# Performance work log

Hardware: AMD Instinct MI355X
Metric: run time of the kernel (lower is better)

## Reference

```python
import jax, jax.numpy as jnp
import numpy as np

NUM_HEADS = 16
BN_EPS = 1e-3  # tf.layers.BatchNormalization default epsilon


def _z_norm(a, axis, scale):
    mu = jnp.mean(a, axis=axis, keepdims=True)
    sd = jnp.std(a, axis=axis, keepdims=True)
    return (a - mu) / (sd * scale + 1e-10)


def setup_inputs() -> dict:
    key = jax.random.key(0)
    ks = jax.random.split(key, 12)
    B, S, D = 4, 1024, 1024
    w = lambda k: jax.random.normal(k, (D, D), dtype=jnp.float32) * 0.02
    return {
        'q': jax.random.normal(ks[0], (B, S, D), dtype=jnp.float32),
        'k': jax.random.normal(ks[1], (B, S, D), dtype=jnp.float32),
        'v': jax.random.normal(ks[2], (B, S, D), dtype=jnp.float32),
        'mask': jax.random.randint(ks[3], (B, 1, S, S), 0, 2, dtype=jnp.int32),
        'is_training': 0,
        'q_gamma': jnp.ones((D,), jnp.float32),
        'q_beta': jnp.zeros((D,), jnp.float32),
        'q_mean': jax.random.normal(ks[4], (D,), dtype=jnp.float32) * 0.1,
        'q_var': jnp.ones((D,), jnp.float32),
        'Wq': w(ks[5]), 'bq': jnp.zeros((D,), jnp.float32),
        'Wqq': w(ks[6]), 'bqq': jnp.zeros((D,), jnp.float32),
        'Wo': w(ks[7]), 'bo': jnp.zeros((D,), jnp.float32),
    }


def reference(q, k, v, mask, is_training, q_gamma, q_beta, q_mean, q_var,
              Wq, bq, Wqq, bqq, Wo, bo):
    B, S, D = q.shape
    H = NUM_HEADS
    dh = D // H
    # BatchNorm (inference mode: call() passes no training flag -> moving stats)
    x = (q - q_mean) * jax.lax.rsqrt(q_var + BN_EPS) * q_gamma + q_beta
    # q = wqq(relu(wq(.)))  (k/v projections are dead: call() sets k = v = q)
    x = jax.nn.relu(x @ Wq + bq)
    x = x @ Wqq + bqq
    qh = x.reshape(B, S, H, dh).transpose(0, 2, 1, 3)  # [B,H,S,dh]
    logits = jnp.einsum('bhqd,bhkd->bhqk', qh, qh) / jnp.sqrt(jnp.float32(dh))
    logits = logits + mask.astype(logits.dtype) * -1e9
    attn = jax.nn.softmax(logits, axis=3)  # [B,H,S,S]
    last = jnp.mean(logits, axis=-1, keepdims=True)        # [B,H,S,1]
    last2 = jnp.mean(logits, axis=(2, 3), keepdims=True)   # [B,H,1,1]
    w_within = jax.nn.softmax(_z_norm(last, 2, 2), axis=2)   # softmax over queries
    w_betw = jax.nn.softmax(_z_norm(last2, 1, 2), axis=1)    # softmax over heads
    attn = attn * w_within * w_betw
    out = jnp.einsum('bhqk,bhkd->bhqd', attn, qh)           # v == qh
    out = out.transpose(0, 2, 1, 3).reshape(B, S, D)
    out = out @ Wo + bo
    return out, attn
```

## Files before the change

kernel.cpp:

```cpp
#include <hip/hip_runtime.h>
#include <math.h>


constexpr int Bz = 4, S = 1024, D = 1024, H = 16, DH = 64;
constexpr int N_ROWS = Bz * S;
#define BN_EPS 1e-3f
#define NEG_BIG -1e9f

typedef __attribute__((ext_vector_type(8))) short bf16x8;
typedef __attribute__((ext_vector_type(8))) unsigned short u16x8;
typedef __attribute__((ext_vector_type(4))) float f32x4;

__device__ inline unsigned short f2bf(float f) {
  union { float f; unsigned int u; } v; v.f = f;
  unsigned int u = v.u;
  return (unsigned short)((u + 0x7FFFu + ((u >> 16) & 1u)) >> 16);
}
__device__ inline float bf2f(unsigned short h) {
  union { unsigned int u; float f; } v; v.u = ((unsigned int)h) << 16;
  return v.f;
}
__device__ inline bf16x8 pack8(float4 a, float4 b) {
  bf16x8 v;
  v[0] = (short)f2bf(a.x); v[1] = (short)f2bf(a.y);
  v[2] = (short)f2bf(a.z); v[3] = (short)f2bf(a.w);
  v[4] = (short)f2bf(b.x); v[5] = (short)f2bf(b.y);
  v[6] = (short)f2bf(b.z); v[7] = (short)f2bf(b.w);
  return v;
}
__device__ inline float4 bnf(float4 f, float4 s, float4 sh) {
  return make_float4(fmaf(f.x, s.x, sh.x), fmaf(f.y, s.y, sh.y),
                     fmaf(f.z, s.z, sh.z), fmaf(f.w, s.w, sh.w));
}

__device__ __forceinline__ void gl16(const void* g, void* l) {
  __builtin_amdgcn_global_load_lds(
      (const __attribute__((address_space(1))) unsigned int*)(unsigned long long)g,
      (__attribute__((address_space(3))) unsigned int*)(unsigned int)(unsigned long long)l,
      16, 0, 0);
}

__global__ __launch_bounds__(256)
void k_prep_all(const float* __restrict__ W0, const float* __restrict__ W1,
                const float* __restrict__ W2, unsigned short* __restrict__ T0,
                unsigned short* __restrict__ T1, unsigned short* __restrict__ T2,
                const float* __restrict__ gamma, const float* __restrict__ beta,
                const float* __restrict__ mean, const float* __restrict__ var,
                float* __restrict__ bnsc, float* __restrict__ bnsh,
                const int* __restrict__ mask, float* __restrict__ n_cnt2,
                float* __restrict__ cs) {
  __shared__ float Ls[64][65];
  const int bid = blockIdx.x, t = threadIdx.x;
  if (bid < 768) {
    const int z = bid >> 8, rem = bid & 255;
    const float* W = z == 0 ? W0 : (z == 1 ? W1 : W2);
    unsigned short* T = z == 0 ? T0 : (z == 1 ? T1 : T2);
    const int k0 = (rem & 15) * 64, n0 = (rem >> 4) * 64;
    {
      const int r = t >> 2, c0 = (t & 3) * 16;
#pragma unroll
      for (int i = 0; i < 4; ++i) {
        float4 f = *(const float4*)&W[(size_t)(k0 + r) * 1024 + n0 + c0 + 4 * i];
        Ls[r][c0 + 4 * i] = f.x; Ls[r][c0 + 4 * i + 1] = f.y;
        Ls[r][c0 + 4 * i + 2] = f.z; Ls[r][c0 + 4 * i + 3] = f.w;
      }
    }
    __syncthreads();
    {
      const int d = t >> 2, c = t & 3;
      u16x8 o0, o1;
#pragma unroll
      for (int i = 0; i < 8; ++i) {
        o0[i] = f2bf(Ls[c * 16 + i][d]);
        o1[i] = f2bf(Ls[c * 16 + 8 + i][d]);
      }
      unsigned short* dst = &T[(size_t)(n0 + d) * 1024 + k0 + c * 16];
      *(u16x8*)dst = o0;
      *(u16x8*)(dst + 8) = o1;
    }
  } else if (bid < 832) {
    const int id = bid - 768;
    const int row = id * 64 + (t >> 2);
    const int4* mp = (const int4*)&mask[(size_t)row * 1024 + (t & 3) * 256];
    int s = 0;
#pragma unroll 8
    for (int i = 0; i < 64; ++i) { int4 m = mp[i]; s += (m.x + m.y) + (m.z + m.w); }
    s += __shfl_xor(s, 1, 64);
    s += __shfl_xor(s, 2, 64);
    if ((t & 3) == 0) n_cnt2[row] = (float)s;
  } else if (bid < 836) {
    const int id = bid - 832;
    *(float4*)&cs[id * 1024 + t * 4] = make_float4(0.f, 0.f, 0.f, 0.f);
  } else {
    const int i = (bid - 836) * 256 + t;
    float sc = gamma[i] * rsqrtf(var[i] + BN_EPS);
    bnsc[i] = sc;
    bnsh[i] = beta[i] - mean[i] * sc;
  }
}

template<int AMODE, bool RELU, bool OUTBF, bool CSUM>
__global__ __launch_bounds__(256)
void k_gemm2n(const void* __restrict__ Asrc, const unsigned short* __restrict__ BT,
              const float* __restrict__ bias, void* __restrict__ C,
              const float* __restrict__ bnsc, const float* __restrict__ bnsh,
              float* __restrict__ cs) {
  __shared__ unsigned short As[128 * 64];
  __shared__ unsigned short Bs[64 * 64];
  const int t = threadIdx.x;
  const int w = t >> 6, l = t & 63, l15 = l & 15, l4 = l >> 4;
  const int m0 = blockIdx.x * 128, n0 = blockIdx.y * 64;
  const int wm = (w >> 1) * 64, wn = (w & 1) * 32;

  f32x4 acc[4][2];
#pragma unroll
  for (int i = 0; i < 4; ++i)
#pragma unroll
    for (int j = 0; j < 2; ++j) acc[i][j] = (f32x4){0.f, 0.f, 0.f, 0.f};

  for (int k0 = 0; k0 < 1024; k0 += 64) {
    __syncthreads();
#pragma unroll
    for (int i = 0; i < 4; ++i) {
      const int c = i * 256 + t, row = c >> 3, slot = c & 7;
      if (AMODE == 0) {
        const char* gs = (const char*)&((const unsigned short*)Asrc)[(size_t)(m0 + row) * 1024 + k0] +
                         ((slot * 16) ^ ((row & 7) << 4));
        gl16(gs, (char*)As + (i * 256 + w * 64) * 16);
      } else {
        const float* ap = &((const float*)Asrc)[(size_t)(m0 + row) * 1024 + k0 + slot * 8];
        float4 f0 = *(const float4*)ap, f1 = *(const float4*)(ap + 4);
        float4 s0 = *(const float4*)&bnsc[k0 + slot * 8];
        float4 s1 = *(const float4*)&bnsc[k0 + slot * 8 + 4];
        float4 h0 = *(const float4*)&bnsh[k0 + slot * 8];
        float4 h1 = *(const float4*)&bnsh[k0 + slot * 8 + 4];
        bf16x8 v = pack8(bnf(f0, s0, h0), bnf(f1, s1, h1));
        *(bf16x8*)((char*)As + row * 128 + ((slot * 16) ^ ((row & 7) << 4))) = v;
      }
    }
#pragma unroll
    for (int i = 0; i < 2; ++i) {
      const int c = i * 256 + t, row = c >> 3, slot = c & 7;
      const char* gs = (const char*)&BT[(size_t)(n0 + row) * 1024 + k0] +
                       ((slot * 16) ^ ((row & 7) << 4));
      gl16(gs, (char*)Bs + (i * 256 + w * 64) * 16);
    }
    __syncthreads();
    bf16x8 af[4][2], bfr[2][2];
#pragma unroll
    for (int bm = 0; bm < 4; ++bm) {
      const int r = wm + bm * 16 + l15;
#pragma unroll
      for (int kk = 0; kk < 2; ++kk)
        af[bm][kk] = *(const bf16x8*)((const char*)As + r * 128 +
                                      ((kk * 64 + l4 * 16) ^ ((r & 7) << 4)));
    }
#pragma unroll
    for (int bn = 0; bn < 2; ++bn) {
      const int r = wn + bn * 16 + l15;
#pragma unroll
      for (int kk = 0; kk < 2; ++kk)
        bfr[bn][kk] = *(const bf16x8*)((const char*)Bs + r * 128 +
                                       ((kk * 64 + l4 * 16) ^ ((r & 7) << 4)));
    }
#pragma unroll
    for (int bm = 0; bm < 4; ++bm)
#pragma unroll
      for (int bn = 0; bn < 2; ++bn) {
        acc[bm][bn] = __builtin_amdgcn_mfma_f32_16x16x32_bf16(af[bm][0], bfr[bn][0], acc[bm][bn], 0, 0, 0);
        acc[bm][bn] = __builtin_amdgcn_mfma_f32_16x16x32_bf16(af[bm][1], bfr[bn][1], acc[bm][bn], 0, 0, 0);
      }
  }
  float bv[2];
#pragma unroll
  for (int bn = 0; bn < 2; ++bn) bv[bn] = bias[n0 + wn + bn * 16 + l15];
  float csum[2] = {0.f, 0.f};
#pragma unroll
  for (int bm = 0; bm < 4; ++bm)
#pragma unroll
    for (int bn = 0; bn < 2; ++bn)
#pragma unroll
      for (int r = 0; r < 4; ++r) {
        float v = acc[bm][bn][r] + bv[bn];
        if (RELU) v = fmaxf(v, 0.f);
        if (CSUM) csum[bn] += v;
        const size_t idx = (size_t)(m0 + wm + bm * 16 + l4 * 4 + r) * 1024 +
                           n0 + wn + bn * 16 + l15;
        if (OUTBF) ((unsigned short*)C)[idx] = f2bf(v);
        else ((float*)C)[idx] = v;
      }
  if (CSUM) {
#pragma unroll
    for (int bn = 0; bn < 2; ++bn) {
      float s = csum[bn];
      s += __shfl_xor(s, 16, 64);
      s += __shfl_xor(s, 32, 64);
      if (l4 == 0)
        atomicAdd(&cs[(m0 >> 10) * 1024 + n0 + wn + bn * 16 + l15], s);
    }
  }
}

__global__ __launch_bounds__(256)
void k_cvt(const unsigned short* __restrict__ xqb, unsigned short* __restrict__ qhT) {
  __shared__ unsigned short Ls[64][72];
  const int t = threadIdx.x;
  const int b = blockIdx.x >> 4;
  const int sb = (blockIdx.x & 15) * 64;
  const int h = blockIdx.y;
  {
    const int r = t >> 2, c0 = (t & 3) * 16;
    const unsigned short* src = &xqb[(size_t)(b * 1024 + sb + r) * 1024 + h * 64 + c0];
    u16x8 a = *(const u16x8*)src;
    u16x8 b8 = *(const u16x8*)(src + 8);
    *(u16x8*)&Ls[r][c0] = a;
    *(u16x8*)&Ls[r][c0 + 8] = b8;
  }
  __syncthreads();
  {
    const int d = t >> 2, c = t & 3;
    u16x8 o0, o1;
#pragma unroll
    for (int i = 0; i < 8; ++i) {
      o0[i] = Ls[c * 16 + i][d];
      o1[i] = Ls[c * 16 + 8 + i][d];
    }
    unsigned short* dst = &qhT[(size_t)((b * 16 + h) * 64 + d) * 1024 + sb + c * 16];
    *(u16x8*)dst = o0;
    *(u16x8*)(dst + 8) = o1;
  }
}

template<int PASS>
__global__ __launch_bounds__(256)
void k_attn6(const unsigned short* __restrict__ xqb, const int* __restrict__ mask,
             const unsigned short* __restrict__ qhT, const float* __restrict__ w_row,
             float* __restrict__ attn, unsigned short* __restrict__ pvb,
             float* __restrict__ denom) {
  __shared__ unsigned short Ks[2][128 * 64];
  __shared__ unsigned short Pst[PASS ? 4 * 16 * 64 : 8];

  const int t = threadIdx.x;
  const int w = t >> 6, l = t & 63;
  const int l15 = l & 15, l4 = l >> 4;
  const int q0 = blockIdx.x * 64;
  const int h = blockIdx.y, b = blockIdx.z;
  const int bh = b * 16 + h;

  bf16x8 qa0, qa1;
  {
    const unsigned short* qp =
        &xqb[(size_t)(b * 1024 + q0 + w * 16 + l15) * 1024 + h * 64 + l4 * 8];
    qa0 = *(const bf16x8*)qp;
    qa1 = *(const bf16x8*)(qp + 32);
  }

  float wsc[4];
  if (PASS == 1) {
#pragma unroll
    for (int r = 0; r < 4; ++r)
      wsc[r] = w_row[(size_t)bh * 1024 + q0 + w * 16 + l4 * 4 + r];
  }

  float dsum[4] = {0.f, 0.f, 0.f, 0.f};
  f32x4 vacc[4];
#pragma unroll
  for (int c = 0; c < 4; ++c) vacc[c] = (f32x4){0.f, 0.f, 0.f, 0.f};

#pragma unroll
  for (int i = 0; i < 4; ++i) {
    const int c = i * 256 + t, row = c >> 3, slot = c & 7;
    const char* gs = (const char*)&xqb[(size_t)(b * 1024 + row) * 1024 + h * 64] +
                     ((slot * 16) ^ ((row & 7) << 4));
    gl16(gs, (char*)Ks[0] + (i * 256 + w * 64) * 16);
  }

  for (int ti = 0; ti < 8; ++ti) {
    __syncthreads();
    const int cur = ti & 1;
    if (ti < 7) {
#pragma unroll
      for (int i = 0; i < 4; ++i) {
        const int c = i * 256 + t, row = c >> 3, slot = c & 7;
        const char* gs = (const char*)&xqb[(size_t)(b * 1024 + (ti + 1) * 128 + row) * 1024 + h * 64] +
                         ((slot * 16) ^ ((row & 7) << 4));
        gl16(gs, (char*)Ks[cur ^ 1] + (i * 256 + w * 64) * 16);
      }
    }
    const int k0 = ti * 128;

#pragma unroll
    for (int half = 0; half < 2; ++half) {
      const int koff = k0 + half * 64;
      f32x4 lacc[4];
#pragma unroll
      for (int c = 0; c < 4; ++c) {
        const int r = half * 64 + c * 16 + l15;
        const char* kb = (const char*)Ks[cur] + r * 128;
        const int rsw = (r & 7) << 4;
        bf16x8 kb0 = *(const bf16x8*)(kb + ((l4 * 16) ^ rsw));
        bf16x8 kb1 = *(const bf16x8*)(kb + ((64 + l4 * 16) ^ rsw));
        f32x4 z = (f32x4){0.f, 0.f, 0.f, 0.f};
        z = __builtin_amdgcn_mfma_f32_16x16x32_bf16(qa0, kb0, z, 0, 0, 0);
        z = __builtin_amdgcn_mfma_f32_16x16x32_bf16(qa1, kb1, z, 0, 0, 0);
        lacc[c] = z;
      }

      int mrr[4][4];
#pragma unroll
      for (int c = 0; c < 4; ++c)
#pragma unroll
        for (int r = 0; r < 4; ++r)
          mrr[c][r] = mask[(size_t)(b * 1024 + q0 + w * 16 + l4 * 4 + r) * 1024 +
                           koff + c * 16 + l15];

#pragma unroll
      for (int c = 0; c < 4; ++c) {
#pragma unroll
        for (int r = 0; r < 4; ++r) {
          float p = __expf(fmaf((float)mrr[c][r], NEG_BIG, lacc[c][r] * 0.125f));
          if (PASS == 0) {
            dsum[r] += p;
          } else {
            attn[(size_t)(bh * 1024 + q0 + w * 16 + l4 * 4 + r) * 1024 +
                 koff + c * 16 + l15] = p * wsc[r];
            const int qq = l4 * 4 + r;
            *(unsigned short*)((char*)&Pst[w * 1024] + qq * 128 +
                               (((c * 16 + l15) * 2) ^ ((qq & 7) << 4))) = f2bf(p);
          }
        }
      }

      if (PASS == 1) {
#pragma unroll
        for (int kk = 0; kk < 2; ++kk) {
          const char* pb = (const char*)&Pst[w * 1024] + l15 * 128;
          bf16x8 pa = *(const bf16x8*)(pb + ((kk * 64 + l4 * 16) ^ ((l15 & 7) << 4)));
#pragma unroll
          for (int c = 0; c < 4; ++c) {
            bf16x8 vb = *(const bf16x8*)&qhT[(size_t)(bh * 64 + c * 16 + l15) * 1024 +
                                             koff + kk * 32 + l4 * 8];
            vacc[c] = __builtin_amdgcn_mfma_f32_16x16x32_bf16(pa, vb, vacc[c], 0, 0, 0);
          }
        }
      }
    }
  }

  if (PASS == 0) {
#pragma unroll
    for (int r = 0; r < 4; ++r) {
      float d2 = dsum[r];
#pragma unroll
      for (int m = 1; m < 16; m <<= 1) d2 += __shfl_xor(d2, m, 64);
      if (l15 == 0)
        denom[(size_t)bh * 1024 + q0 + w * 16 + l4 * 4 + r] = d2;
    }
  } else {
#pragma unroll
    for (int c = 0; c < 4; ++c)
#pragma unroll
      for (int r = 0; r < 4; ++r)
        pvb[(size_t)(b * 1024 + q0 + w * 16 + l4 * 4 + r) * 1024 +
            h * 64 + c * 16 + l15] = f2bf(vacc[c][r] * wsc[r]);
  }
}

__global__ __launch_bounds__(256)
void k_wwithin(const unsigned short* __restrict__ xqb, const float* __restrict__ cs,
               const float* __restrict__ n_cnt2, const float* __restrict__ denom,
               float* __restrict__ w_row) {
  __shared__ double buf[1024];
  __shared__ double red[256];
  __shared__ float csl[64];
  __shared__ double sh_mu, sh_sd, sh_zm, sh_es;
  const int bh = blockIdx.x, t = threadIdx.x;
  const int base = bh << 10;
  const int b = bh >> 4, h = bh & 15;
  const int nbase = b << 10;
  if (t < 64) csl[t] = cs[b * 1024 + h * 64 + t];
  __syncthreads();
  double part = 0;
  for (int j = 0; j < 4; ++j) {
    const int q2 = t + j * 256;
    const unsigned short* xr = &xqb[(size_t)(b * 1024 + q2) * 1024 + h * 64];
    float s = 0.f;
#pragma unroll
    for (int dd = 0; dd < 64; dd += 8) {
      u16x8 xv = *(const u16x8*)&xr[dd];
      s += bf2f(xv[0]) * csl[dd]     + bf2f(xv[1]) * csl[dd + 1] +
           bf2f(xv[2]) * csl[dd + 2] + bf2f(xv[3]) * csl[dd + 3] +
           bf2f(xv[4]) * csl[dd + 4] + bf2f(xv[5]) * csl[dd + 5] +
           bf2f(xv[6]) * csl[dd + 6] + bf2f(xv[7]) * csl[dd + 7];
    }
    double last = ((double)(s * 0.125f) - 1e9 * (double)n_cnt2[nbase + q2]) * (1.0 / 1024.0);
    buf[q2] = last; part += last;
  }
  red[t] = part; __syncthreads();
  for (int s2 = 128; s2 > 0; s2 >>= 1) { if (t < s2) red[t] += red[t + s2]; __syncthreads(); }
  if (t == 0) sh_mu = red[0] * (1.0 / 1024.0);
  __syncthreads();
  const double mu = sh_mu;
  part = 0;
  for (int q2 = t; q2 < 1024; q2 += 256) { double d = buf[q2] - mu; part += d * d; }
  red[t] = part; __syncthreads();
  for (int s2 = 128; s2 > 0; s2 >>= 1) { if (t < s2) red[t] += red[t + s2]; __syncthreads(); }
  if (t == 0) sh_sd = sqrt(red[0] * (1.0 / 1024.0));
  __syncthreads();
  const double dn = sh_sd * 2.0 + 1e-10;
  part = -1e300;
  for (int q2 = t; q2 < 1024; q2 += 256) {
    double z = (buf[q2] - mu) / dn;
    buf[q2] = z;
    part = fmax(part, z);
  }
  red[t] = part; __syncthreads();
  for (int s2 = 128; s2 > 0; s2 >>= 1) { if (t < s2) red[t] = fmax(red[t], red[t + s2]); __syncthreads(); }
  if (t == 0) sh_zm = red[0];
  __syncthreads();
  const double zm = sh_zm;
  part = 0;
  for (int q2 = t; q2 < 1024; q2 += 256) {
    double e = exp(buf[q2] - zm);
    buf[q2] = e; part += e;
  }
  red[t] = part; __syncthreads();
  for (int s2 = 128; s2 > 0; s2 >>= 1) { if (t < s2) red[t] += red[t + s2]; __syncthreads(); }
  if (t == 0) sh_es = red[0];
  __syncthreads();
  const double tot = sh_es;
  for (int q2 = t; q2 < 1024; q2 += 256) {
    w_row[base + q2] = (float)(buf[q2] / tot * 0.0625 / (double)denom[base + q2]);
  }
}

extern "C" void kernel_launch(void* const* d_in, const int* in_sizes, int n_in,
                              void* d_out, int out_size, void* d_ws, size_t ws_size,
                              hipStream_t stream) {
  const float* q      = (const float*)d_in[0];
  const int*   mask   = (const int*)d_in[3];
  const float* q_gamma = (const float*)d_in[5];
  const float* q_beta  = (const float*)d_in[6];
  const float* q_mean  = (const float*)d_in[7];
  const float* q_var   = (const float*)d_in[8];
  const float* Wq  = (const float*)d_in[9];
  const float* bq  = (const float*)d_in[10];
  const float* Wqq = (const float*)d_in[11];
  const float* bqq = (const float*)d_in[12];
  const float* Wo  = (const float*)d_in[13];
  const float* bo  = (const float*)d_in[14];

  float* out  = (float*)d_out;
  float* attn = (float*)d_out + (size_t)N_ROWS * D;
  unsigned short* xqb = (unsigned short*)d_out;

  char* ws = (char*)d_ws;
  unsigned short* x1b = (unsigned short*)(ws);
  unsigned short* qhT = (unsigned short*)(ws + (8u << 20));
  unsigned short* pvb = (unsigned short*)(ws + (16u << 20));
  unsigned short* WqT  = (unsigned short*)(ws + (32u << 20));
  unsigned short* WqqT = (unsigned short*)(ws + (34u << 20));
  unsigned short* WoT  = (unsigned short*)(ws + (36u << 20));
  float* cs     = (float*)(ws + (38u << 20));
  float* denom  = cs + 4096;
  float* w_row  = denom + 65536;
  float* n_cnt2 = w_row + 65536;
  float* bnsc   = n_cnt2 + 4096;
  float* bnsh   = bnsc + 1024;

  k_prep_all<<<840, 256, 0, stream>>>(Wq, Wqq, Wo, WqT, WqqT, WoT,
                                      q_gamma, q_beta, q_mean, q_var, bnsc, bnsh,
                                      mask, n_cnt2, cs);

  dim3 gg(32, 16);
  k_gemm2n<1, true, true, false><<<gg, 256, 0, stream>>>(q, WqT, bq, x1b, bnsc, bnsh, nullptr);
  k_gemm2n<0, false, true, true><<<gg, 256, 0, stream>>>(x1b, WqqT, bqq, xqb, nullptr, nullptr, cs);

  k_cvt<<<dim3(64, 16), 256, 0, stream>>>(xqb, qhT);

  dim3 ga(16, 16, 4);
  k_attn6<0><<<ga, 256, 0, stream>>>(xqb, mask, nullptr, nullptr, nullptr, nullptr, denom);
  k_wwithin<<<Bz * H, 256, 0, stream>>>(xqb, cs, n_cnt2, denom, w_row);
  k_attn6<1><<<ga, 256, 0, stream>>>(xqb, mask, qhT, w_row, attn, pvb, nullptr);

  k_gemm2n<0, false, false, false><<<gg, 256, 0, stream>>>(pvb, WoT, bo, out, nullptr, nullptr, nullptr);
}
```

Baseline: 246.4 us.

## Materialize bf16 softmax numerators in pass one and reuse them for the attn write and PV

```diff
diff --git a/kernel.cpp b/kernel.cpp
--- a/kernel.cpp
+++ b/kernel.cpp
@@ -231,14 +231,11 @@
   }
 }
 
-template<int PASS>
 __global__ __launch_bounds__(256)
-void k_attn6(const unsigned short* __restrict__ xqb, const int* __restrict__ mask,
-             const unsigned short* __restrict__ qhT, const float* __restrict__ w_row,
-             float* __restrict__ attn, unsigned short* __restrict__ pvb,
-             float* __restrict__ denom) {
+void k_attn7(const unsigned short* __restrict__ xqb, const int* __restrict__ mask,
+             unsigned short* __restrict__ pbuf, float* __restrict__ denom) {
   __shared__ unsigned short Ks[2][128 * 64];
-  __shared__ unsigned short Pst[PASS ? 4 * 16 * 64 : 8];
+  __shared__ unsigned short Pst[4 * 16 * 64];
 
   const int t = threadIdx.x;
   const int w = t >> 6, l = t & 63;
@@ -255,17 +252,10 @@
     qa1 = *(const bf16x8*)(qp + 32);
   }
 
-  float wsc[4];
-  if (PASS == 1) {
-#pragma unroll
-    for (int r = 0; r < 4; ++r)
-      wsc[r] = w_row[(size_t)bh * 1024 + q0 + w * 16 + l4 * 4 + r];
-  }
-
   float dsum[4] = {0.f, 0.f, 0.f, 0.f};
-  f32x4 vacc[4];
-#pragma unroll
-  for (int c = 0; c < 4; ++c) vacc[c] = (f32x4){0.f, 0.f, 0.f, 0.f};
+
+  const int prow = l >> 2, pc = l & 3;
+  const size_t pbase = ((size_t)bh << 20) + (size_t)(q0 + w * 16 + prow) * 1024;
 
 #pragma unroll
   for (int i = 0; i < 4; ++i) {
@@ -319,51 +309,97 @@
 #pragma unroll
         for (int r = 0; r < 4; ++r) {
           float p = __expf(fmaf((float)mrr[c][r], NEG_BIG, lacc[c][r] * 0.125f));
-          if (PASS == 0) {
-            dsum[r] += p;
-          } else {
-            attn[(size_t)(bh * 1024 + q0 + w * 16 + l4 * 4 + r) * 1024 +
-                 koff + c * 16 + l15] = p * wsc[r];
-            const int qq = l4 * 4 + r;
-            *(unsigned short*)((char*)&Pst[w * 1024] + qq * 128 +
-                               (((c * 16 + l15) * 2) ^ ((qq & 7) << 4))) = f2bf(p);
-          }
+          dsum[r] += p;
+          const int qq = l4 * 4 + r;
+          *(unsigned short*)((char*)&Pst[w * 1024] + qq * 128 +
+                             (((c * 16 + l15) * 2) ^ ((qq & 7) << 4))) = f2bf(p);
         }
       }
 
-      if (PASS == 1) {
-#pragma unroll
-        for (int kk = 0; kk < 2; ++kk) {
-          const char* pb = (const char*)&Pst[w * 1024] + l15 * 128;
-          bf16x8 pa = *(const bf16x8*)(pb + ((kk * 64 + l4 * 16) ^ ((l15 & 7) << 4)));
-#pragma unroll
-          for (int c = 0; c < 4; ++c) {
-            bf16x8 vb = *(const bf16x8*)&qhT[(size_t)(bh * 64 + c * 16 + l15) * 1024 +
-                                             koff + kk * 32 + l4 * 8];
-            vacc[c] = __builtin_amdgcn_mfma_f32_16x16x32_bf16(pa, vb, vacc[c], 0, 0, 0);
-          }
-        }
-      }
-    }
-  }
-
-  if (PASS == 0) {
-#pragma unroll
-    for (int r = 0; r < 4; ++r) {
-      float d2 = dsum[r];
-#pragma unroll
-      for (int m = 1; m < 16; m <<= 1) d2 += __shfl_xor(d2, m, 64);
-      if (l15 == 0)
-        denom[(size_t)bh * 1024 + q0 + w * 16 + l4 * 4 + r] = d2;
-    }
-  } else {
-#pragma unroll
-    for (int c = 0; c < 4; ++c)
-#pragma unroll
-      for (int r = 0; r < 4; ++r)
-        pvb[(size_t)(b * 1024 + q0 + w * 16 + l4 * 4 + r) * 1024 +
-            h * 64 + c * 16 + l15] = f2bf(vacc[c][r] * wsc[r]);
-  }
+      {
+        const char* pb = (const char*)&Pst[w * 1024] + prow * 128;
+        const int psw = (prow & 7) << 4;
+        bf16x8 p0 = *(const bf16x8*)(pb + ((pc * 32) ^ psw));
+        bf16x8 p1 = *(const bf16x8*)(pb + ((pc * 32 + 16) ^ psw));
+        unsigned short* pd = &pbuf[pbase + koff + pc * 16];
+        *(bf16x8*)pd = p0;
+        *(bf16x8*)(pd + 8) = p1;
+      }
+    }
+  }
+
+#pragma unroll
+  for (int r = 0; r < 4; ++r) {
+    float d2 = dsum[r];
+#pragma unroll
+    for (int m = 1; m < 16; m <<= 1) d2 += __shfl_xor(d2, m, 64);
+    if (l15 == 0)
+      denom[(size_t)bh * 1024 + q0 + w * 16 + l4 * 4 + r] = d2;
+  }
+}
+
+__global__ __launch_bounds__(256)
+void k_attn_pv(const unsigned short* __restrict__ pbuf,
+               const unsigned short* __restrict__ qhT, const float* __restrict__ w_row,
+               float* __restrict__ attn, unsigned short* __restrict__ pvb) {
+  __shared__ unsigned short Pst[4 * 16 * 64];
+
+  const int t = threadIdx.x;
+  const int w = t >> 6, l = t & 63;
+  const int l15 = l & 15, l4 = l >> 4;
+  const int q0 = blockIdx.x * 64;
+  const int h = blockIdx.y, b = blockIdx.z;
+  const int bh = b * 16 + h;
+
+  const int prow = l >> 2, pc = l & 3;
+  const float wq = w_row[(size_t)bh * 1024 + q0 + w * 16 + prow];
+  float wsc[4];
+#pragma unroll
+  for (int r = 0; r < 4; ++r)
+    wsc[r] = w_row[(size_t)bh * 1024 + q0 + w * 16 + l4 * 4 + r];
+
+  f32x4 vacc[4];
+#pragma unroll
+  for (int c = 0; c < 4; ++c) vacc[c] = (f32x4){0.f, 0.f, 0.f, 0.f};
+
+  const size_t pbase = ((size_t)bh << 20) + (size_t)(q0 + w * 16 + prow) * 1024;
+  const size_t abase = ((size_t)bh * 1024 + q0 + w * 16 + prow) * 1024;
+  char* pdst = (char*)&Pst[w * 1024] + prow * 128;
+  const int psw = (prow & 7) << 4;
+
+  for (int k0 = 0; k0 < 1024; k0 += 64) {
+    bf16x8 p0 = *(const bf16x8*)&pbuf[pbase + k0 + pc * 16];
+    bf16x8 p1 = *(const bf16x8*)&pbuf[pbase + k0 + pc * 16 + 8];
+    float* ap = &attn[abase + k0 + pc * 16];
+    *(float4*)ap = make_float4(bf2f((unsigned short)p0[0]) * wq, bf2f((unsigned short)p0[1]) * wq,
+                               bf2f((unsigned short)p0[2]) * wq, bf2f((unsigned short)p0[3]) * wq);
+    *(float4*)(ap + 4) = make_float4(bf2f((unsigned short)p0[4]) * wq, bf2f((unsigned short)p0[5]) * wq,
+                                     bf2f((unsigned short)p0[6]) * wq, bf2f((unsigned short)p0[7]) * wq);
+    *(float4*)(ap + 8) = make_float4(bf2f((unsigned short)p1[0]) * wq, bf2f((unsigned short)p1[1]) * wq,
+                                     bf2f((unsigned short)p1[2]) * wq, bf2f((unsigned short)p1[3]) * wq);
+    *(float4*)(ap + 12) = make_float4(bf2f((unsigned short)p1[4]) * wq, bf2f((unsigned short)p1[5]) * wq,
+                                      bf2f((unsigned short)p1[6]) * wq, bf2f((unsigned short)p1[7]) * wq);
+    *(bf16x8*)(pdst + ((pc * 32) ^ psw)) = p0;
+    *(bf16x8*)(pdst + ((pc * 32 + 16) ^ psw)) = p1;
+#pragma unroll
+    for (int kk = 0; kk < 2; ++kk) {
+      const char* pb2 = (const char*)&Pst[w * 1024] + l15 * 128;
+      bf16x8 pa = *(const bf16x8*)(pb2 + ((kk * 64 + l4 * 16) ^ ((l15 & 7) << 4)));
+#pragma unroll
+      for (int c = 0; c < 4; ++c) {
+        bf16x8 vb = *(const bf16x8*)&qhT[(size_t)(bh * 64 + c * 16 + l15) * 1024 +
+                                         k0 + kk * 32 + l4 * 8];
+        vacc[c] = __builtin_amdgcn_mfma_f32_16x16x32_bf16(pa, vb, vacc[c], 0, 0, 0);
+      }
+    }
+  }
+
+#pragma unroll
+  for (int c = 0; c < 4; ++c)
+#pragma unroll
+    for (int r = 0; r < 4; ++r)
+      pvb[(size_t)(b * 1024 + q0 + w * 16 + l4 * 4 + r) * 1024 +
+          h * 64 + c * 16 + l15] = f2bf(vacc[c][r] * wsc[r]);
 }
 
 __global__ __launch_bounds__(256)
@@ -467,6 +503,7 @@
   float* n_cnt2 = w_row + 65536;
   float* bnsc   = n_cnt2 + 4096;
   float* bnsh   = bnsc + 1024;
+  unsigned short* pbuf = (unsigned short*)(ws + (64ull << 20));
 
   k_prep_all<<<840, 256, 0, stream>>>(Wq, Wqq, Wo, WqT, WqqT, WoT,
                                       q_gamma, q_beta, q_mean, q_var, bnsc, bnsh,
@@ -479,9 +516,9 @@
   k_cvt<<<dim3(64, 16), 256, 0, stream>>>(xqb, qhT);
 
   dim3 ga(16, 16, 4);
-  k_attn6<0><<<ga, 256, 0, stream>>>(xqb, mask, nullptr, nullptr, nullptr, nullptr, denom);
+  k_attn7<<<ga, 256, 0, stream>>>(xqb, mask, pbuf, denom);
   k_wwithin<<<Bz * H, 256, 0, stream>>>(xqb, cs, n_cnt2, denom, w_row);
-  k_attn6<1><<<ga, 256, 0, stream>>>(xqb, mask, qhT, w_row, attn, pvb, nullptr);
+  k_attn_pv<<<ga, 256, 0, stream>>>(pbuf, qhT, w_row, attn, pvb);
 
   k_gemm2n<0, false, false, false><<<gg, 256, 0, stream>>>(pvb, WoT, bo, out, nullptr, nullptr, nullptr);
 }
```

New measurement: 312.0 us. +26.6%, slower.
